# Kernel tuning notes

Measured on AMD Instinct MI355X. Metric: run time of the kernel, lower is better.

Reference implementation:

```python
import jax, jax.numpy as jnp
import numpy as np

N, LD, LM, D = 8, 1024, 1024, 1024
H = 16
HS = D // H  # 64

def setup_inputs() -> dict:
    key = jax.random.key(0)
    k1, k2, k3 = jax.random.split(key, 3)
    inp = jax.random.normal(k1, (N, LD, D), dtype=jnp.float32)
    mem = jax.random.normal(k2, (N, LM, D), dtype=jnp.float32)
    mask = jnp.ones((N, LM), dtype=jnp.float32)
    Wc = jax.random.normal(k3, (D, 2 * D), dtype=jnp.float32) * 0.02
    bc = jnp.zeros((D,), dtype=jnp.float32)
    return {"input": inp, "memory": mem, "mask": mask, "Wc": Wc, "bc": bc}

def reference(input, memory, mask, Wc, bc):
    # split heads: [N, L, D] -> [N, H, L, HS]
    q = input.reshape(N, LD, H, HS).transpose(0, 2, 1, 3)
    k = memory.reshape(N, LM, H, HS).transpose(0, 2, 1, 3)
    v = k
    scores = jnp.einsum('bhqd,bhkd->bhqk', q, k) / jnp.sqrt(jnp.float32(HS))
    # additive key-padding mask: -1e30 * (1 - mask), broadcast over heads & queries
    scores = scores + (-1e30) * (1.0 - mask[:, None, None, :])
    probs = jax.nn.softmax(scores, axis=-1)
    ctx = jnp.einsum('bhqk,bhkd->bhqd', probs, v)
    ctx = ctx.transpose(0, 2, 1, 3).reshape(N, LD, D)
    out = jnp.concatenate([input, ctx], axis=-1) @ Wc.T + bc
    return jax.nn.sigmoid(out) * jnp.tanh(out)
```

## Files before the change

kernel.cpp:

```cpp
#include <hip/hip_runtime.h>

#define NB 8
#define LSEQ 1024
#define DMODEL 1024
#define NH 16
#define HS 64
#define KX 2048

#define LOG2E 1.44269504f

typedef __bf16 bf16_t;
typedef __attribute__((ext_vector_type(4))) __bf16 bf16x4;
typedef __attribute__((ext_vector_type(8))) __bf16 bf16x8;
typedef __attribute__((ext_vector_type(4))) float floatx4;

typedef __attribute__((address_space(3))) unsigned int lds_u32;
typedef const __attribute__((address_space(1))) unsigned int glob_u32;

__device__ __forceinline__ floatx4 mfma16(bf16x8 a, bf16x8 b, floatx4 c) {
    return __builtin_amdgcn_mfma_f32_16x16x32_bf16(a, b, c, 0, 0, 0);
}
__device__ __forceinline__ void gl_lds16(const bf16_t* g, bf16_t* l) {
    __builtin_amdgcn_global_load_lds((glob_u32*)g, (lds_u32*)l, 16, 0, 0);
}

__global__ __launch_bounds__(256) void prep_kernel(
        const float* __restrict__ inp, const float* __restrict__ mem,
        const float* __restrict__ Wc, const float* __restrict__ mask,
        bf16_t* __restrict__ Xb, bf16_t* __restrict__ Mb,
        bf16_t* __restrict__ Wb, bf16_t* __restrict__ VTg,
        float* __restrict__ biasG) {
    __shared__ bf16_t Tl[64][72];
    const int tid = threadIdx.x;
    const int b = blockIdx.x;
    if (b < 2048) {
        const int kb = b & 15;
        const int h  = (b >> 4) & 15;
        const int n  = b >> 8;
        {
            const int key = tid >> 2, seg = tid & 3;
            const float* src = mem + ((size_t)(n * LSEQ + kb * 64 + key)) * DMODEL + h * HS + seg * 16;
            floatx4 f[4];
#pragma unroll
            for (int j = 0; j < 4; ++j) f[j] = *(const floatx4*)(src + j * 4);
            bf16x8 w0, w1;
#pragma unroll
            for (int j = 0; j < 8; ++j) { w0[j] = (bf16_t)f[j >> 2][j & 3]; w1[j] = (bf16_t)f[2 + (j >> 2)][j & 3]; }
            bf16_t* d = &Tl[key][seg * 16];
            *(bf16x8*)d = w0;
            *(bf16x8*)(d + 8) = w1;
            bf16_t* md = Mb + ((size_t)(n * LSEQ + kb * 64 + key)) * DMODEL + h * HS + seg * 16;
            *(bf16x8*)md = w0;
            *(bf16x8*)(md + 8) = w1;
        }
        __syncthreads();
        {
            const int dim = tid >> 2, ks = tid & 3;
            bf16x8 w0, w1;
#pragma unroll
            for (int j = 0; j < 8; ++j) { w0[j] = Tl[ks * 16 + j][dim]; w1[j] = Tl[ks * 16 + 8 + j][dim]; }
            bf16_t* dst = VTg + ((size_t)((n * NH + h) * HS + dim)) * LSEQ + kb * 64 + ks * 16;
            *(bf16x8*)dst = w0;
            *(bf16x8*)(dst + 8) = w1;
        }
    } else if (b < 6144) {
        const size_t i8 = ((size_t)(b - 2048) * 256 + tid) * 8;
        floatx4 f0 = *(const floatx4*)(inp + i8);
        floatx4 f1 = *(const floatx4*)(inp + i8 + 4);
        bf16x8 w;
#pragma unroll
        for (int j = 0; j < 4; ++j) { w[j] = (bf16_t)f0[j]; w[4 + j] = (bf16_t)f1[j]; }
        *(bf16x8*)(Xb + (i8 >> 10) * KX + (i8 & 1023)) = w;
    } else if (b < 7168) {
        const size_t i8 = ((size_t)(b - 6144) * 256 + tid) * 8;
        floatx4 f0 = *(const floatx4*)(Wc + i8);
        floatx4 f1 = *(const floatx4*)(Wc + i8 + 4);
        bf16x8 w;
#pragma unroll
        for (int j = 0; j < 4; ++j) { w[j] = (bf16_t)f0[j]; w[4 + j] = (bf16_t)f1[j]; }
        *(bf16x8*)(Wb + i8) = w;
    } else {
        const size_t i4 = ((size_t)(b - 7168) * 256 + tid) * 4;
        floatx4 mv = *(const floatx4*)(mask + i4);
        floatx4 o;
#pragma unroll
        for (int j = 0; j < 4; ++j) o[j] = (-1e30f * (1.0f - mv[j]) - 8.0f) * LOG2E;
        *(floatx4*)(biasG + i4) = o;
    }
}

__global__ __launch_bounds__(256) void attn_kernel(
        bf16_t* __restrict__ Xb, const bf16_t* __restrict__ Mb,
        const bf16_t* __restrict__ VTg, const float* __restrict__ biasG) {
    __shared__ __align__(16) bf16_t Kl[128 * 64];
    __shared__ __align__(16) bf16_t Vl[64 * 128];
    __shared__ __align__(16) bf16_t Pl[4 * 1024];

    const int tid  = threadIdx.x;
    const int lane = tid & 63;
    const int wv   = tid >> 6;
    const int ln15 = lane & 15;
    const int quad = lane >> 4;

    const int bid = blockIdx.x;
    const int nh  = bid & 127;
    const int qt  = bid >> 7;
    const int h   = nh & 15;
    const int n   = nh >> 4;
    const int q0  = qt * 128 + wv * 32;

    bf16x8 qf[2][2];
#pragma unroll
    for (int nt = 0; nt < 2; ++nt) {
        const bf16_t* qp = Xb + ((size_t)(n * LSEQ + q0 + nt * 16 + ln15)) * KX + h * HS;
#pragma unroll
        for (int kk = 0; kk < 2; ++kk) {
            bf16x8 r = *(const bf16x8*)(qp + kk * 32 + quad * 8);
            bf16x8 a;
#pragma unroll
            for (int j = 0; j < 8; ++j) a[j] = (bf16_t)((float)r[j] * (0.125f * LOG2E));
            qf[nt][kk] = a;
        }
    }

    bf16x8 ones;
#pragma unroll
    for (int j = 0; j < 8; ++j) ones[j] = (bf16_t)1.0f;

    floatx4 ot[4][2];
    floatx4 lacc[2];
#pragma unroll
    for (int md = 0; md < 4; ++md)
#pragma unroll
        for (int nt = 0; nt < 2; ++nt) ot[md][nt] = (floatx4){0.f, 0.f, 0.f, 0.f};
#pragma unroll
    for (int nt = 0; nt < 2; ++nt) lacc[nt] = (floatx4){0.f, 0.f, 0.f, 0.f};

    bf16_t* myP = &Pl[wv * 1024];
    const int qm = ln15 & 6;

    for (int kt = 0; kt < LSEQ / 128; ++kt) {
        const int kb = kt * 128;
        __syncthreads();
#pragma unroll
        for (int i = 0; i < 4; ++i) {
            const int kbase = wv * 32 + i * 8;
            const int key = kbase + (lane >> 3), s = lane & 7, g = s ^ (key & 7);
            gl_lds16(Mb + ((size_t)(n * LSEQ + kb + key)) * DMODEL + h * HS + g * 8,
                     &Kl[kbase * 64]);
        }
#pragma unroll
        for (int i = 0; i < 4; ++i) {
            const int dbase = wv * 16 + i * 4;
            const int dim = dbase + (lane >> 4), s = lane & 15, g = s ^ (dim & 7);
            gl_lds16(VTg + ((size_t)((n * NH + h) * HS + dim)) * LSEQ + kb + g * 8,
                     &Vl[dbase * 128]);
        }
        __syncthreads();

#pragma unroll
        for (int half = 0; half < 2; ++half) {
            floatx4 s4[4][2];
#pragma unroll
            for (int m = 0; m < 4; ++m) {
                const int key = half * 64 + m * 16 + ln15;
                floatx4 b4 = *(const floatx4*)(biasG + n * LSEQ + kb + half * 64 + m * 16 + quad * 4);
#pragma unroll
                for (int nt = 0; nt < 2; ++nt) s4[m][nt] = b4;
#pragma unroll
                for (int kk = 0; kk < 2; ++kk) {
                    const int slot = (kk * 4 + quad) ^ (ln15 & 7);
                    bf16x8 a = *(const bf16x8*)(&Kl[key * 64 + slot * 8]);
#pragma unroll
                    for (int nt = 0; nt < 2; ++nt) s4[m][nt] = mfma16(a, qf[nt][kk], s4[m][nt]);
                }
            }
#pragma unroll
            for (int m = 0; m < 4; ++m)
#pragma unroll
                for (int nt = 0; nt < 2; ++nt)
#pragma unroll
                    for (int reg = 0; reg < 4; ++reg)
                        s4[m][nt][reg] = __builtin_amdgcn_exp2f(s4[m][nt][reg]);

#pragma unroll
            for (int c = 0; c < 2; ++c) {
#pragma unroll
                for (int mm = 0; mm < 2; ++mm) {
                    const int m = c * 2 + mm;
                    const int gsl = ((mm * 4 + quad) ^ qm) * 4;
#pragma unroll
                    for (int nt = 0; nt < 2; ++nt) {
                        const int q = nt * 16 + ln15;
                        bf16x4 p;
#pragma unroll
                        for (int reg = 0; reg < 4; ++reg) p[reg] = (bf16_t)s4[m][nt][reg];
                        *(bf16x4*)(&myP[q * 32 + gsl]) = p;
                    }
                }
                const int cglob = half * 2 + c;
                bf16x8 pb[2];
#pragma unroll
                for (int nt = 0; nt < 2; ++nt) {
                    const int q = nt * 16 + ln15;
                    const int s16 = quad ^ (qm >> 1);
                    pb[nt] = *(const bf16x8*)(&myP[q * 32 + s16 * 8]);
                    lacc[nt] = mfma16(ones, pb[nt], lacc[nt]);
                }
#pragma unroll
                for (int md = 0; md < 4; ++md) {
                    const int d = md * 16 + ln15;
                    const int vslot = (cglob * 4 + quad) ^ (d & 7);
                    bf16x8 va = *(const bf16x8*)(&Vl[d * 128 + vslot * 8]);
#pragma unroll
                    for (int nt = 0; nt < 2; ++nt) ot[md][nt] = mfma16(va, pb[nt], ot[md][nt]);
                }
            }
        }
    }

#pragma unroll
    for (int nt = 0; nt < 2; ++nt) {
        const float inv = 1.0f / lacc[nt][0];
        const int q = q0 + nt * 16 + ln15;
        bf16_t* op = Xb + ((size_t)(n * LSEQ + q)) * KX + DMODEL + h * HS;
#pragma unroll
        for (int md = 0; md < 4; ++md) {
            bf16x4 w;
#pragma unroll
            for (int reg = 0; reg < 4; ++reg) w[reg] = (bf16_t)(ot[md][nt][reg] * inv);
            *(bf16x4*)(op + md * 16 + quad * 4) = w;
        }
    }
}

__global__ __launch_bounds__(256, 4) void gemm_kernel(
        const bf16_t* __restrict__ Xb, const bf16_t* __restrict__ Wb,
        const float* __restrict__ bc, float* __restrict__ out) {
    __shared__ __align__(16) bf16_t Al[128 * 64];
    __shared__ __align__(16) bf16_t Bl[64 * 64];

    const int tid  = threadIdx.x;
    const int lane = tid & 63;
    const int wv   = tid >> 6;
    const int ln15 = lane & 15;
    const int quad = lane >> 4;

    const int bm = blockIdx.x & 63;
    const int bn = blockIdx.x >> 6;
    const int mbase = bm * 128, nbase = bn * 64;

    floatx4 acc[2][4];
#pragma unroll
    for (int i = 0; i < 2; ++i)
#pragma unroll
        for (int j = 0; j < 4; ++j) acc[i][j] = (floatx4){0.f, 0.f, 0.f, 0.f};

    for (int it = 0; it < KX / 64; ++it) {
        const int k0 = it * 64;
        __syncthreads();
#pragma unroll
        for (int i = 0; i < 4; ++i) {
            const int r0  = i * 32 + wv * 8;
            const int row = r0 + (lane >> 3);
            const int g   = (lane & 7) ^ (row & 7);
            gl_lds16(Xb + (size_t)(mbase + row) * KX + k0 + g * 8, &Al[r0 * 64]);
        }
#pragma unroll
        for (int j = 0; j < 2; ++j) {
            const int r0  = j * 32 + wv * 8;
            const int row = r0 + (lane >> 3);
            const int g   = (lane & 7) ^ (row & 7);
            gl_lds16(Wb + (size_t)(nbase + row) * KX + k0 + g * 8, &Bl[r0 * 64]);
        }
        __syncthreads();

#pragma unroll
        for (int kk = 0; kk < 2; ++kk) {
            bf16x8 af[2], bfr[4];
#pragma unroll
            for (int mi = 0; mi < 2; ++mi) {
                const int row = wv * 32 + mi * 16 + ln15;
                const int slot = (kk * 4 + quad) ^ (row & 7);
                af[mi] = *(const bf16x8*)(&Al[row * 64 + slot * 8]);
            }
#pragma unroll
            for (int ni = 0; ni < 4; ++ni) {
                const int row = ni * 16 + ln15;
                const int slot = (kk * 4 + quad) ^ (row & 7);
                bfr[ni] = *(const bf16x8*)(&Bl[row * 64 + slot * 8]);
            }
#pragma unroll
            for (int mi = 0; mi < 2; ++mi)
#pragma unroll
                for (int ni = 0; ni < 4; ++ni)
                    acc[mi][ni] = mfma16(af[mi], bfr[ni], acc[mi][ni]);
        }
    }

#pragma unroll
    for (int ni = 0; ni < 4; ++ni) {
        const int col = nbase + ni * 16 + ln15;
        const float b = bc[col];
#pragma unroll
        for (int mi = 0; mi < 2; ++mi) {
#pragma unroll
            for (int reg = 0; reg < 4; ++reg) {
                const int row = mbase + wv * 32 + mi * 16 + quad * 4 + reg;
                const float z  = acc[mi][ni][reg] + b;
                const float sg = 1.0f / (1.0f + __expf(-z));
                const float th = 2.0f / (1.0f + __expf(-2.0f * z)) - 1.0f;
                out[(size_t)row * 1024 + col] = sg * th;
            }
        }
    }
}

extern "C" void kernel_launch(void* const* d_in, const int* in_sizes, int n_in,
                              void* d_out, int out_size, void* d_ws, size_t ws_size,
                              hipStream_t stream) {
    const float* inp  = (const float*)d_in[0];
    const float* mem  = (const float*)d_in[1];
    const float* mask = (const float*)d_in[2];
    const float* Wc   = (const float*)d_in[3];
    const float* bc   = (const float*)d_in[4];
    float* out = (float*)d_out;

    bf16_t* Xb  = (bf16_t*)d_ws;
    bf16_t* Mb  = Xb + (size_t)8192 * 2048;
    bf16_t* Wb  = Mb + (size_t)8192 * 1024;
    bf16_t* VTg = Wb + (size_t)1024 * 2048;
    float* biasG = (float*)(VTg + (size_t)8192 * 1024);

    prep_kernel<<<7176, 256, 0, stream>>>(inp, mem, Wc, mask, Xb, Mb, Wb, VTg, biasG);
    attn_kernel<<<NB * NH * (LSEQ / 128), 256, 0, stream>>>(Xb, Mb, VTg, biasG);
    gemm_kernel<<<(8192 / 128) * (1024 / 64), 256, 0, stream>>>(Xb, Wb, bc, out);
}
```

Before: 225.0 us.

## Double-buffer K and V LDS tiles to overlap global loads with compute

Splits the K and V shared-memory tiles into two buffers. The first tile is loaded before the loop, and each iteration issues async global-to-LDS loads for the next tile while computing on the current one. This removes one barrier per iteration and is meant to hide memory latency behind the MFMA work. In exchange LDS use per block grows, which can lower occupancy. The compiler may also insert conservative vmcnt waits before the LDS reads, which would cancel the overlap.

Result: no change. 220.9 us (-1.8%).

```diff
diff --git a/kernel.cpp b/kernel.cpp
--- a/kernel.cpp
+++ b/kernel.cpp
@@ -92,8 +92,8 @@
 __global__ __launch_bounds__(256) void attn_kernel(
         bf16_t* __restrict__ Xb, const bf16_t* __restrict__ Mb,
         const bf16_t* __restrict__ VTg, const float* __restrict__ biasG) {
-    __shared__ __align__(16) bf16_t Kl[128 * 64];
-    __shared__ __align__(16) bf16_t Vl[64 * 128];
+    __shared__ __align__(16) bf16_t Kl[2][128 * 64];
+    __shared__ __align__(16) bf16_t Vl[2][64 * 128];
     __shared__ __align__(16) bf16_t Pl[4 * 1024];
 
     const int tid  = threadIdx.x;
@@ -109,6 +109,11 @@
     const int n   = nh >> 4;
     const int q0  = qt * 128 + wv * 32;
 
+    const int kst_base = wv * 32;
+    const int vst_base = wv * 16;
+    const bf16_t* Mbase = Mb + ((size_t)(n * LSEQ)) * DMODEL + h * HS;
+    const bf16_t* Vbase = VTg + ((size_t)((n * NH + h) * HS)) * LSEQ;
+
     bf16x8 qf[2][2];
 #pragma unroll
     for (int nt = 0; nt < 2; ++nt) {
@@ -139,24 +144,42 @@
     bf16_t* myP = &Pl[wv * 1024];
     const int qm = ln15 & 6;
 
+    {
+        const int kb = 0;
+#pragma unroll
+        for (int i = 0; i < 4; ++i) {
+            const int kbase = kst_base + i * 8;
+            const int key = kbase + (lane >> 3), s = lane & 7, g = s ^ (key & 7);
+            gl_lds16(Mbase + ((size_t)(kb + key)) * DMODEL + g * 8, &Kl[0][kbase * 64]);
+        }
+#pragma unroll
+        for (int i = 0; i < 4; ++i) {
+            const int dbase = vst_base + i * 4;
+            const int dim = dbase + (lane >> 4), s = lane & 15, g = s ^ (dim & 7);
+            gl_lds16(Vbase + ((size_t)dim) * LSEQ + kb + g * 8, &Vl[0][dbase * 128]);
+        }
+    }
+
     for (int kt = 0; kt < LSEQ / 128; ++kt) {
         const int kb = kt * 128;
+        const int cur = kt & 1;
         __syncthreads();
-#pragma unroll
-        for (int i = 0; i < 4; ++i) {
-            const int kbase = wv * 32 + i * 8;
-            const int key = kbase + (lane >> 3), s = lane & 7, g = s ^ (key & 7);
-            gl_lds16(Mb + ((size_t)(n * LSEQ + kb + key)) * DMODEL + h * HS + g * 8,
-                     &Kl[kbase * 64]);
-        }
-#pragma unroll
-        for (int i = 0; i < 4; ++i) {
-            const int dbase = wv * 16 + i * 4;
-            const int dim = dbase + (lane >> 4), s = lane & 15, g = s ^ (dim & 7);
-            gl_lds16(VTg + ((size_t)((n * NH + h) * HS + dim)) * LSEQ + kb + g * 8,
-                     &Vl[dbase * 128]);
-        }
-        __syncthreads();
+
+        if (kt < LSEQ / 128 - 1) {
+            const int kb1 = kb + 128;
+#pragma unroll
+            for (int i = 0; i < 4; ++i) {
+                const int kbase = kst_base + i * 8;
+                const int key = kbase + (lane >> 3), s = lane & 7, g = s ^ (key & 7);
+                gl_lds16(Mbase + ((size_t)(kb1 + key)) * DMODEL + g * 8, &Kl[cur ^ 1][kbase * 64]);
+            }
+#pragma unroll
+            for (int i = 0; i < 4; ++i) {
+                const int dbase = vst_base + i * 4;
+                const int dim = dbase + (lane >> 4), s = lane & 15, g = s ^ (dim & 7);
+                gl_lds16(Vbase + ((size_t)dim) * LSEQ + kb1 + g * 8, &Vl[cur ^ 1][dbase * 128]);
+            }
+        }
 
 #pragma unroll
         for (int half = 0; half < 2; ++half) {
@@ -170,7 +193,7 @@
 #pragma unroll
                 for (int kk = 0; kk < 2; ++kk) {
                     const int slot = (kk * 4 + quad) ^ (ln15 & 7);
-                    bf16x8 a = *(const bf16x8*)(&Kl[key * 64 + slot * 8]);
+                    bf16x8 a = *(const bf16x8*)(&Kl[cur][key * 64 + slot * 8]);
 #pragma unroll
                     for (int nt = 0; nt < 2; ++nt) s4[m][nt] = mfma16(a, qf[nt][kk], s4[m][nt]);
                 }
@@ -211,7 +234,7 @@
                 for (int md = 0; md < 4; ++md) {
                     const int d = md * 16 + ln15;
                     const int vslot = (cglob * 4 + quad) ^ (d & 7);
-                    bf16x8 va = *(const bf16x8*)(&Vl[d * 128 + vslot * 8]);
+                    bf16x8 va = *(const bf16x8*)(&Vl[cur][d * 128 + vslot * 8]);
 #pragma unroll
                     for (int nt = 0; nt < 2; ++nt) ot[md][nt] = mfma16(va, pb[nt], ot[md][nt]);
                 }
```

## Split attention tile loop into full QK/exp phase then full PV phase

Applied to the files above, without the earlier changes.

Restructures the per-tile loop so both halves of scores are computed, exponentiated and written to a larger per-wave P buffer first, then a second pass runs all P·V MFMAs. P storage grows to 32 KB per block with a new swizzle, and K/V base pointers are hoisted out of the loop. The aim is to separate the exp/convert work from the PV MFMA chain and remove the within-half store/load dependency on a shared small buffer. The cost is higher LDS use, which may reduce occupancy.

After: 222.9 us. No clear change (-0.9%).

```diff
diff --git a/kernel.cpp b/kernel.cpp
--- a/kernel.cpp
+++ b/kernel.cpp
@@ -94,7 +94,7 @@
         const bf16_t* __restrict__ VTg, const float* __restrict__ biasG) {
     __shared__ __align__(16) bf16_t Kl[128 * 64];
     __shared__ __align__(16) bf16_t Vl[64 * 128];
-    __shared__ __align__(16) bf16_t Pl[4 * 1024];
+    __shared__ __align__(16) bf16_t Pl[8 * 2048];
 
     const int tid  = threadIdx.x;
     const int lane = tid & 63;
@@ -109,6 +109,9 @@
     const int n   = nh >> 4;
     const int q0  = qt * 128 + wv * 32;
 
+    const bf16_t* Mbase = Mb + ((size_t)(n * LSEQ)) * DMODEL + h * HS;
+    const bf16_t* Vbase = VTg + ((size_t)((n * NH + h) * HS)) * LSEQ;
+
     bf16x8 qf[2][2];
 #pragma unroll
     for (int nt = 0; nt < 2; ++nt) {
@@ -136,8 +139,7 @@
 #pragma unroll
     for (int nt = 0; nt < 2; ++nt) lacc[nt] = (floatx4){0.f, 0.f, 0.f, 0.f};
 
-    bf16_t* myP = &Pl[wv * 1024];
-    const int qm = ln15 & 6;
+    const int qm7 = ln15 & 7;
 
     for (int kt = 0; kt < LSEQ / 128; ++kt) {
         const int kb = kt * 128;
@@ -146,15 +148,13 @@
         for (int i = 0; i < 4; ++i) {
             const int kbase = wv * 32 + i * 8;
             const int key = kbase + (lane >> 3), s = lane & 7, g = s ^ (key & 7);
-            gl_lds16(Mb + ((size_t)(n * LSEQ + kb + key)) * DMODEL + h * HS + g * 8,
-                     &Kl[kbase * 64]);
+            gl_lds16(Mbase + ((size_t)(kb + key)) * DMODEL + g * 8, &Kl[kbase * 64]);
         }
 #pragma unroll
         for (int i = 0; i < 4; ++i) {
             const int dbase = wv * 16 + i * 4;
             const int dim = dbase + (lane >> 4), s = lane & 15, g = s ^ (dim & 7);
-            gl_lds16(VTg + ((size_t)((n * NH + h) * HS + dim)) * LSEQ + kb + g * 8,
-                     &Vl[dbase * 128]);
+            gl_lds16(Vbase + ((size_t)dim) * LSEQ + kb + g * 8, &Vl[dbase * 128]);
         }
         __syncthreads();
 
@@ -169,7 +169,7 @@
                 for (int nt = 0; nt < 2; ++nt) s4[m][nt] = b4;
 #pragma unroll
                 for (int kk = 0; kk < 2; ++kk) {
-                    const int slot = (kk * 4 + quad) ^ (ln15 & 7);
+                    const int slot = (kk * 4 + quad) ^ qm7;
                     bf16x8 a = *(const bf16x8*)(&Kl[key * 64 + slot * 8]);
 #pragma unroll
                     for (int nt = 0; nt < 2; ++nt) s4[m][nt] = mfma16(a, qf[nt][kk], s4[m][nt]);
@@ -183,34 +183,39 @@
                     for (int reg = 0; reg < 4; ++reg)
                         s4[m][nt][reg] = __builtin_amdgcn_exp2f(s4[m][nt][reg]);
 
-#pragma unroll
-            for (int c = 0; c < 2; ++c) {
-#pragma unroll
-                for (int mm = 0; mm < 2; ++mm) {
-                    const int m = c * 2 + mm;
-                    const int gsl = ((mm * 4 + quad) ^ qm) * 4;
-#pragma unroll
-                    for (int nt = 0; nt < 2; ++nt) {
-                        const int q = nt * 16 + ln15;
-                        bf16x4 p;
-#pragma unroll
-                        for (int reg = 0; reg < 4; ++reg) p[reg] = (bf16_t)s4[m][nt][reg];
-                        *(bf16x4*)(&myP[q * 32 + gsl]) = p;
-                    }
-                }
-                const int cglob = half * 2 + c;
-                bf16x8 pb[2];
+            bf16_t* myPh = &Pl[(wv * 2 + half) * 2048];
+#pragma unroll
+            for (int m = 0; m < 4; ++m) {
+                const int hs = m * 4 + quad;
+                const int s  = hs >> 1;
 #pragma unroll
                 for (int nt = 0; nt < 2; ++nt) {
                     const int q = nt * 16 + ln15;
-                    const int s16 = quad ^ (qm >> 1);
-                    pb[nt] = *(const bf16x8*)(&myP[q * 32 + s16 * 8]);
+                    bf16x4 p;
+#pragma unroll
+                    for (int reg = 0; reg < 4; ++reg) p[reg] = (bf16_t)s4[m][nt][reg];
+                    *(bf16x4*)(&myPh[q * 64 + (s ^ (q & 7)) * 8 + (hs & 1) * 4]) = p;
+                }
+            }
+        }
+
+#pragma unroll
+        for (int half = 0; half < 2; ++half) {
+            bf16_t* myPh = &Pl[(wv * 2 + half) * 2048];
+#pragma unroll
+            for (int kkh = 0; kkh < 2; ++kkh) {
+                bf16x8 pb[2];
+#pragma unroll
+                for (int nt = 0; nt < 2; ++nt) {
+                    const int q = nt * 16 + ln15;
+                    const int slot = (kkh * 4 + quad) ^ (q & 7);
+                    pb[nt] = *(const bf16x8*)(&myPh[q * 64 + slot * 8]);
                     lacc[nt] = mfma16(ones, pb[nt], lacc[nt]);
                 }
 #pragma unroll
                 for (int md = 0; md < 4; ++md) {
                     const int d = md * 16 + ln15;
-                    const int vslot = (cglob * 4 + quad) ^ (d & 7);
+                    const int vslot = (half * 8 + kkh * 4 + quad) ^ (d & 7);
                     bf16x8 va = *(const bf16x8*)(&Vl[d * 128 + vslot * 8]);
 #pragma unroll
                     for (int nt = 0; nt < 2; ++nt) ot[md][nt] = mfma16(va, pb[nt], ot[md][nt]);
```
